# Performance work log

Measured on AMD Instinct MI355X. Metric: run time of the kernel, lower is better.

Reference implementation:

```python
import jax, jax.numpy as jnp
import numpy as np

B, R, C, O, I = 256, 1152, 10, 16, 8  # batch, routes, digit caps, out dim, in dim


def conv2d(x, w, b, stride, pad):
    y = jax.lax.conv_general_dilated(
        x, w, (stride, stride), ((pad, pad), (pad, pad)),
        dimension_numbers=("NCHW", "OIHW", "NCHW"))
    return y + b[None, :, None, None]


def maxpool2(x):
    # kernel 2, stride 2, padding 1 (torch pads with -inf for max pool)
    return jax.lax.reduce_window(
        x, -jnp.inf, jax.lax.max,
        (1, 1, 2, 2), (1, 1, 2, 2), ((0, 0), (0, 0), (1, 1), (1, 1)))


def squash(t):
    sn = (t ** 2).sum(-1, keepdims=True)
    return sn * t / ((1.0 + sn) * jnp.sqrt(sn))


def setup_inputs() -> dict:
    key = jax.random.key(0)
    ks = jax.random.split(key, 8)
    return {
        "data": jax.random.normal(ks[0], (B, 3, 76, 76), dtype=jnp.float32),
        "conv1_w": jax.random.normal(ks[1], (64, 3, 3, 3), dtype=jnp.float32) * 0.1,
        "conv1_b": jnp.zeros((64,), jnp.float32),
        "conv2_w": jax.random.normal(ks[2], (128, 64, 3, 3), dtype=jnp.float32) * 0.05,
        "conv2_b": jnp.zeros((128,), jnp.float32),
        "prim_w": jax.random.normal(ks[3], (8, 32, 128, 9, 9), dtype=jnp.float32) * 0.02,
        "prim_b": jnp.zeros((8, 32), jnp.float32),
        "W": jax.random.normal(ks[4], (R, C, O, I), dtype=jnp.float32),
        "cls_w1": jax.random.normal(ks[5], (10, 160, 100), dtype=jnp.float32) * 0.05,
        "cls_b1": jnp.zeros((10, 100), jnp.float32),
        "cls_w2": jax.random.normal(ks[6], (10, 100, 1), dtype=jnp.float32) * 0.05,
        "cls_b2": jnp.zeros((10, 1), jnp.float32),
    }


def reference(data, conv1_w, conv1_b, conv2_w, conv2_b, prim_w, prim_b, W,
              cls_w1, cls_b1, cls_w2, cls_b2):
    # ---- ConvLayer ----
    x = jax.nn.relu(conv2d(data, conv1_w, conv1_b, 1, 0))   # [B,64,74,74]
    x = maxpool2(x)                                          # [B,64,38,38]
    x = jax.nn.relu(conv2d(x, conv2_w, conv2_b, 1, 1))       # [B,128,38,38]
    x = maxpool2(x)                                          # [B,128,20,20]

    # ---- PrimaryCaps: 8 parallel convs fused into one grouped-by-output conv ----
    pw = prim_w.reshape(8 * 32, 128, 9, 9)
    pb = prim_b.reshape(8 * 32)
    u = conv2d(x, pw, pb, 2, 0)                              # [B,256,6,6]
    u = u.reshape(B, R, I)                                   # [B,1152,8] (same flatten order as torch view)
    u = squash(u)

    # ---- DigitCaps dynamic routing ----
    u_hat = jnp.einsum("rcoi,bri->brco", W, u)               # [B,R,C,O]
    b_ij = jnp.zeros((R, C), u_hat.dtype)
    v_j = None
    for it in range(3):
        c_ij = jax.nn.softmax(b_ij, axis=0)                  # softmax over routes (dim=1 in torch)
        s_j = jnp.einsum("rc,brco->bco", c_ij, u_hat)        # [B,C,O]
        # torch squashes over trailing singleton dim -> elementwise squash
        v_j = squash(s_j[..., None])[..., 0]                 # [B,C,O]
        if it < 2:
            a_ij = jnp.einsum("brco,bco->brc", u_hat, v_j).mean(0)  # [R,C]
            b_ij = b_ij + a_ij

    output = v_j[..., None]                                  # [B,10,16,1]

    # ---- 10 classifiers (Linear->ReLU->Linear->Sigmoid), batched over classifier idx k ----
    feat = output.reshape(B, -1)                             # [B,160]
    h = jax.nn.relu(jnp.einsum("bf,kfh->bkh", feat, cls_w1) + cls_b1)
    logits = jnp.einsum("bkh,kho->bko", h, cls_w2) + cls_b2  # [B,10,1]
    cls = jax.nn.sigmoid(logits)[..., 0]                     # [B,10]
    return (output, cls)
```

## Files before the change

kernel.cpp:

```cpp
#include <hip/hip_runtime.h>
#include <hip/hip_bf16.h>


typedef __bf16 bf16x8 __attribute__((ext_vector_type(8)));
typedef float  f32x4  __attribute__((ext_vector_type(4)));
typedef ushort u16x8  __attribute__((ext_vector_type(8)));

static __device__ __forceinline__ ushort f2bf(float f) {
    __hip_bfloat16 h = __float2bfloat16(f);
    return *(ushort*)&h;
}
static __device__ __forceinline__ float b2f(ushort u) {
    return __uint_as_float(((unsigned)u) << 16);
}

typedef __attribute__((address_space(1))) const unsigned int* as1_u32p;
typedef __attribute__((address_space(3))) unsigned int* as3_u32p;
static __device__ __forceinline__ void gl16(const void* g, void* l) {
    __builtin_amdgcn_global_load_lds((as1_u32p)g, (as3_u32p)l, 16, 0, 0);
}

__global__ __launch_bounds__(256) void k_prep_awt(
    const float* __restrict__ pw, __hip_bfloat16* __restrict__ Awt)
{
    __shared__ float ls[10368];
    const int oc = blockIdx.x;
    const int tid = threadIdx.x;
    const float* src = pw + oc * 10368;
    for (int i = tid; i < 10368; i += 256) ls[i] = src[i];
    __syncthreads();
    __hip_bfloat16* dst = Awt + oc * 10368;
    for (int o = tid; o < 10368; o += 256) {
        int k81 = o >> 7, ic = o & 127;
        dst[o] = __float2bfloat16(ls[ic * 81 + k81]);
    }
}

__global__ __launch_bounds__(256) void k_prep_wt(
    const float* __restrict__ W, __hip_bfloat16* __restrict__ Wt)
{
    __shared__ float ls[8 * 1281];
    const int r0 = blockIdx.x * 8;
    const int tid = threadIdx.x;
    const float* src = W + (size_t)r0 * 1280;
    for (int i = tid; i < 10240; i += 256) {
        int rr = i / 1280, rem = i - rr * 1280;
        ls[rr * 1281 + rem] = src[i];
    }
    __syncthreads();
    for (int o = tid; o < 10240; o += 256) {
        int co = o >> 6, rem = o & 63;
        int rr = rem >> 3, i = rem & 7;
        Wt[(size_t)co * 9216 + r0 * 8 + rem] =
            __float2bfloat16(ls[rr * 1281 + co * 8 + i]);
    }
}

__global__ __launch_bounds__(256) void k_prep_small(
    const float* __restrict__ w1, const float* __restrict__ w2,
    __hip_bfloat16* __restrict__ Aw1, __hip_bfloat16* __restrict__ Aw2)
{
    int t = blockIdx.x * 256 + threadIdx.x;
    if (t < 73728) {
        int oc = t / 576, rem = t % 576;
        int k9 = rem >> 6, ic = rem & 63;
        Aw2[t] = __float2bfloat16(w2[(oc * 64 + ic) * 9 + k9]);
    } else if (t < 75776) {
        int q = t - 73728;
        int oc = q >> 5, k = q & 31;
        Aw1[q] = __float2bfloat16(k < 27 ? w1[oc * 27 + k] : 0.f);
    }
}

__global__ __launch_bounds__(256) void k_conv1_mfma(
    const float* __restrict__ data, const __hip_bfloat16* __restrict__ Aw1,
    const float* __restrict__ b1, __hip_bfloat16* __restrict__ P1t)
{
    __shared__ float tile[960];
    const int tid = threadIdx.x;
    const int py = blockIdx.x % 38, b = blockIdx.x / 38;

    #pragma unroll
    for (int c = 0; c < 4; c++) {
        int idx = tid + c * 256;
        if (idx < 960) {
            float val = 0.f;
            if (idx < 936) {
                int ic = idx / 312, rem = idx % 312;
                int rl = rem / 78, lc = rem % 78;
                int ri = 2 * py - 1 + rl, xi = lc - 1;
                if ((unsigned)ri < 76u && (unsigned)xi < 76u)
                    val = data[(b * 3 + ic) * 5776 + ri * 76 + xi];
            }
            tile[idx] = val;
        }
    }

    const int wave = tid >> 6, lane = tid & 63;
    const int l15 = lane & 15, quad = lane >> 4;

    bf16x8 af = *(const bf16x8*)((const ushort*)Aw1 + (wave * 16 + l15) * 32 + quad * 8);

    int koff[8]; bool kok[8];
    #pragma unroll
    for (int j = 0; j < 8; j++) {
        int kk = quad * 8 + j;
        kok[j] = kk < 27;
        int ic = kk / 9, rem = kk - ic * 9, ky = rem / 3, kx = rem - ky * 3;
        koff[j] = kok[j] ? (ic * 312 + ky * 78 + kx) : 0;
    }

    float bias[4];
    #pragma unroll
    for (int r = 0; r < 4; r++) bias[r] = b1[wave * 16 + quad * 4 + r];

    const bool valid0 = (py > 0);
    const bool valid1 = (py < 37);

    __syncthreads();

    #pragma unroll
    for (int t5 = 0; t5 < 5; t5++) {
        int n_x = t5 * 16 + l15;
        bool col_ok = (unsigned)(n_x - 1) < 74u;

        bf16x8 bf0, bf1;
        #pragma unroll
        for (int j = 0; j < 8; j++) {
            float v0 = tile[koff[j] + n_x];
            float v1 = tile[koff[j] + 78 + n_x];
            bool ok = col_ok && kok[j];
            bf0[j] = (__bf16)(ok ? v0 : 0.f);
            bf1[j] = (__bf16)(ok ? v1 : 0.f);
        }
        f32x4 z = {0.f, 0.f, 0.f, 0.f};
        f32x4 c0 = __builtin_amdgcn_mfma_f32_16x16x32_bf16(af, bf0, z, 0, 0, 0);
        f32x4 c1 = __builtin_amdgcn_mfma_f32_16x16x32_bf16(af, bf1, z, 0, 0, 0);

        f32x4 p;
        #pragma unroll
        for (int r = 0; r < 4; r++) {
            float r0 = (valid0 && col_ok) ? fmaxf(c0[r] + bias[r], 0.f) : 0.f;
            float r1 = (valid1 && col_ok) ? fmaxf(c1[r] + bias[r], 0.f) : 0.f;
            p[r] = fmaxf(r0, r1);
        }
        #pragma unroll
        for (int r = 0; r < 4; r++)
            p[r] = fmaxf(p[r], __shfl_xor(p[r], 1));

        if (!(l15 & 1)) {
            int px = t5 * 8 + (l15 >> 1);
            if (px < 38) {
                ushort4 pk;
                pk.x = f2bf(p[0]); pk.y = f2bf(p[1]);
                pk.z = f2bf(p[2]); pk.w = f2bf(p[3]);
                *(ushort4*)((ushort*)P1t + ((size_t)(b * 38 + py) * 38 + px) * 64
                            + wave * 16 + quad * 4) = pk;
            }
        }
    }
}

__global__ __launch_bounds__(256, 4) void k_conv2_pool_mfma(
    const __hip_bfloat16* __restrict__ P1t,
    const __hip_bfloat16* __restrict__ Aw2,
    const float* __restrict__ cb,
    const ushort* __restrict__ zpage,
    __hip_bfloat16* __restrict__ P2t)
{
    __shared__ ushort lA[128 * 64];
    __shared__ ushort lB[128 * 64];
    const int tid  = threadIdx.x;
    const int grp  = blockIdx.x / 50, toff = blockIdx.x % 50;
    const int wave = tid >> 6, lane = tid & 63;
    const int wm   = wave & 1, wn = wave >> 1;
    const int lane15 = lane & 15, quad = lane >> 4;

    const int sl = ((lane & 7) ^ (lane >> 3)) * 8;

    int oA[4], oB[4], yv[4], xv[4];
    #pragma unroll
    for (int i = 0; i < 4; i++) {
        int row = wave * 32 + i * 8 + (lane >> 3);
        oA[i] = row * 576 + sl;
        int off = toff * 128 + row;
        int bb = off / 1600, rem = off % 1600;
        int cell = rem >> 2, q = rem & 3;
        int py = cell / 20, px = cell % 20;
        int y = 2 * py - 1 + (q >> 1), x = 2 * px - 1 + (q & 1);
        yv[i] = y; xv[i] = x;
        oB[i] = (((grp * 4 + bb) * 38 + (y - 1)) * 38 + (x - 1)) * 64 + sl;
    }
    ushort* lAq = &lA[wave * 2048];
    ushort* lBq = &lB[wave * 2048];

    const int s7 = lane15 & 7;
    const int c0 = (quad ^ s7) * 8;
    const int c1 = ((quad + 4) ^ s7) * 8;
    const ushort* aRd0 = &lA[(wm * 64 + lane15) * 64 + c0];
    const ushort* aRd1 = &lA[(wm * 64 + lane15) * 64 + c1];
    const ushort* bRd0 = &lB[(wn * 64 + lane15) * 64 + c0];
    const ushort* bRd1 = &lB[(wn * 64 + lane15) * 64 + c1];

    f32x4 zero = {0.f, 0.f, 0.f, 0.f};
    f32x4 acc[4][4];
    #pragma unroll
    for (int i = 0; i < 4; i++)
        #pragma unroll
        for (int j = 0; j < 4; j++) acc[i][j] = zero;

    for (int kb = 0; kb < 9; kb++) {
        int ky = kb / 3, kx = kb - ky * 3;
        int dB = (ky * 38 + kx) << 6;
        int dA = kb << 6;

        __syncthreads();
        #pragma unroll
        for (int i = 0; i < 4; i++) {
            gl16((const ushort*)Aw2 + oA[i] + dA, lAq + i * 512);
            bool ok = ((unsigned)(yv[i] - 1 + ky) < 38u) &&
                      ((unsigned)(xv[i] - 1 + kx) < 38u);
            const ushort* src = ok ? ((const ushort*)P1t + (ptrdiff_t)(oB[i] + dB))
                                   : (zpage + sl);
            gl16(src, lBq + i * 512);
        }
        __syncthreads();

        #pragma unroll
        for (int kk = 0; kk < 2; kk++) {
            const ushort* ap = kk ? aRd1 : aRd0;
            const ushort* bp = kk ? bRd1 : bRd0;
            bf16x8 af[4], bf[4];
            #pragma unroll
            for (int tm = 0; tm < 4; tm++)
                af[tm] = *(const bf16x8*)(ap + tm * 1024);
            #pragma unroll
            for (int tn = 0; tn < 4; tn++)
                bf[tn] = *(const bf16x8*)(bp + tn * 1024);
            #pragma unroll
            for (int tm = 0; tm < 4; tm++)
                #pragma unroll
                for (int tn = 0; tn < 4; tn++)
                    acc[tm][tn] = __builtin_amdgcn_mfma_f32_16x16x32_bf16(
                        af[tm], bf[tn], acc[tm][tn], 0, 0, 0);
        }
    }

    #pragma unroll
    for (int tn = 0; tn < 4; tn++) {
        int woff = toff * 128 + wn * 64 + tn * 16 + lane15;
        int ebb = woff / 1600, erem = woff % 1600;
        int ecell = erem >> 2, eq = erem & 3;
        int epy = ecell / 20, epx = ecell % 20;
        int ey = 2 * epy - 1 + (eq >> 1), ex = 2 * epx - 1 + (eq & 1);
        bool vq = ((unsigned)ey < 38u) && ((unsigned)ex < 38u);
        int eb = grp * 4 + ebb;
        #pragma unroll
        for (int tm = 0; tm < 4; tm++) {
            int m0 = wm * 64 + tm * 16 + quad * 4;
            f32x4 a = acc[tm][tn];
            f32x4 p;
            #pragma unroll
            for (int r = 0; r < 4; r++)
                p[r] = vq ? fmaxf(a[r] + cb[m0 + r], 0.f) : 0.f;
            #pragma unroll
            for (int r = 0; r < 4; r++) {
                p[r] = fmaxf(p[r], __shfl_xor(p[r], 1));
                p[r] = fmaxf(p[r], __shfl_xor(p[r], 2));
            }
            if (eq == 0) {
                ushort4 pk;
                pk.x = f2bf(p[0]); pk.y = f2bf(p[1]);
                pk.z = f2bf(p[2]); pk.w = f2bf(p[3]);
                *(ushort4*)((ushort*)P2t + (((size_t)eb * 20 + epy) * 20 + epx) * 128 + m0) = pk;
            }
        }
    }
}

__global__ __launch_bounds__(256, 4) void k_primcaps_mfma(
    const __hip_bfloat16* __restrict__ P2t,
    const __hip_bfloat16* __restrict__ Awt,
    float* __restrict__ partU)
{
    __shared__ ushort lA[128 * 64];
    __shared__ ushort lB[128 * 64];
    const int tid  = threadIdx.x;
    const int chunk = blockIdx.x / 144;
    const int tile  = blockIdx.x % 144;
    const int bm   = tile & 1;
    const int bn   = tile >> 1;
    const int wave = tid >> 6, lane = tid & 63;
    const int wm   = wave & 1, wn = wave >> 1;
    const int lane15 = lane & 15, quad = lane >> 4;

    const int sl = ((lane & 7) ^ (lane >> 3)) * 8;

    int oA[4], oB[4];
    #pragma unroll
    for (int i = 0; i < 4; i++) {
        int row = wave * 32 + i * 8 + (lane >> 3);
        oA[i] = (bm * 128 + row) * 10368 + sl;
        int n = bn * 128 + row;
        int cbn = n / 36, cs = n % 36;
        int cy = cs / 6, cx = cs % 6;
        oB[i] = ((cbn * 20 + 2 * cy) * 20 + 2 * cx) * 128 + sl;
    }
    ushort* lAq = &lA[wave * 2048];
    ushort* lBq = &lB[wave * 2048];

    const int s7 = lane15 & 7;
    const int c0 = (quad ^ s7) * 8;
    const int c1 = ((quad + 4) ^ s7) * 8;
    const ushort* aRd0 = &lA[(wm * 64 + lane15) * 64 + c0];
    const ushort* aRd1 = &lA[(wm * 64 + lane15) * 64 + c1];
    const ushort* bRd0 = &lB[(wn * 64 + lane15) * 64 + c0];
    const ushort* bRd1 = &lB[(wn * 64 + lane15) * 64 + c1];

    f32x4 zero = {0.f, 0.f, 0.f, 0.f};
    f32x4 acc[4][4];
    #pragma unroll
    for (int i = 0; i < 4; i++)
        #pragma unroll
        for (int j = 0; j < 4; j++) acc[i][j] = zero;

    const int kb0 = chunk * 27;
    for (int ki = 0; ki < 27; ki++) {
        int kb = kb0 + ki;
        int k81 = kb >> 1;
        int ky = k81 / 9, kx = k81 - ky * 9;
        int dB = (ky * 20 + kx) * 128 + (kb & 1) * 64;
        int dA = kb << 6;

        __syncthreads();
        #pragma unroll
        for (int i = 0; i < 4; i++) {
            gl16((const ushort*)Awt + (size_t)oA[i] + dA, lAq + i * 512);
            gl16((const ushort*)P2t + oB[i] + dB, lBq + i * 512);
        }
        __syncthreads();

        #pragma unroll
        for (int kk = 0; kk < 2; kk++) {
            const ushort* ap = kk ? aRd1 : aRd0;
            const ushort* bp = kk ? bRd1 : bRd0;
            bf16x8 af[4], bf[4];
            #pragma unroll
            for (int tm = 0; tm < 4; tm++)
                af[tm] = *(const bf16x8*)(ap + tm * 1024);
            #pragma unroll
            for (int tn = 0; tn < 4; tn++)
                bf[tn] = *(const bf16x8*)(bp + tn * 1024);
            #pragma unroll
            for (int tm = 0; tm < 4; tm++)
                #pragma unroll
                for (int tn = 0; tn < 4; tn++)
                    acc[tm][tn] = __builtin_amdgcn_mfma_f32_16x16x32_bf16(
                        af[tm], bf[tn], acc[tm][tn], 0, 0, 0);
        }
    }

    float* base = partU + chunk * 2359296;
    #pragma unroll
    for (int tm = 0; tm < 4; tm++) {
        int m0 = bm * 128 + wm * 64 + tm * 16 + quad * 4;
        #pragma unroll
        for (int tn = 0; tn < 4; tn++) {
            int nn = bn * 128 + wn * 64 + tn * 16 + lane15;
            int ob = nn / 36, os = nn % 36;
            float* up = base + ob * 9216 + os;
            f32x4 a = acc[tm][tn];
            #pragma unroll
            for (int r = 0; r < 4; r++)
                up[(m0 + r) * 36] = a[r];
        }
    }
}

__global__ __launch_bounds__(256) void k_reduce_squash(
    const float* __restrict__ partU, const float* __restrict__ pb,
    ushort* __restrict__ u_bf)
{
    int t = blockIdx.x * 256 + threadIdx.x;
    float4 a = {0.f, 0.f, 0.f, 0.f}, b4 = {0.f, 0.f, 0.f, 0.f};
    #pragma unroll
    for (int p = 0; p < 6; p++) {
        const float4* pp = (const float4*)(partU + p * 2359296 + t * 8);
        float4 x = pp[0], y = pp[1];
        a.x += x.x; a.y += x.y; a.z += x.z; a.w += x.w;
        b4.x += y.x; b4.y += y.y; b4.z += y.z; b4.w += y.w;
    }
    int lb = (t % 1152) * 8;
    int oc0 = lb / 36, s0 = lb - oc0 * 36;
    float vals[8] = {a.x, a.y, a.z, a.w, b4.x, b4.y, b4.z, b4.w};
    float sn = 0.f;
    #pragma unroll
    for (int e = 0; e < 8; e++) {
        int oc = oc0 + ((s0 + e) >= 36 ? 1 : 0);
        vals[e] += pb[oc];
        sn += vals[e] * vals[e];
    }
    float sc = sqrtf(sn) / (1.f + sn);
    u16x8 o8;
    #pragma unroll
    for (int e = 0; e < 8; e++) o8[e] = f2bf(vals[e] * sc);
    *(u16x8*)(u_bf + (size_t)t * 8) = o8;
}

__global__ __launch_bounds__(320) void k_sj_fused(
    const ushort* __restrict__ u_bf,
    const __hip_bfloat16* __restrict__ Wt,
    const float* __restrict__ expb,
    float* __restrict__ partS,
    int iter)
{
    __shared__ ushort ush[8 * 576];
    __shared__ float cf[720];
    __shared__ float sred[320];
    __shared__ float sinv[10];
    const int tid = threadIdx.x;
    const int bt = blockIdx.x & 31, kc = blockIdx.x >> 5;
    const int co = tid % 160, half = tid / 160;

    if (iter > 0) {
        int c = tid % 10, g = tid / 10;
        float s = 0.f;
        for (int r = g; r < 1152; r += 32) s += expb[r * 10 + c];
        sred[tid] = s;
        for (int i = tid; i < 720; i += 320) cf[i] = expb[kc * 720 + i];
        __syncthreads();
        if (tid < 10) {
            float t2 = 0.f;
            #pragma unroll
            for (int gg = 0; gg < 32; gg++) t2 += sred[tid + gg * 10];
            sinv[tid] = 1.f / t2;
        }
    }
    for (int i = tid; i < 576; i += 320)
        ((uint4*)ush)[i] = ((const uint4*)u_bf)[(size_t)(bt * 8 + (i / 72)) * 1152
                                                + kc * 72 + (i % 72)];
    __syncthreads();

    const int cc = co >> 4;
    const float scl = (iter > 0) ? sinv[cc] : 0.f;
    const float cuni = 1.f / 1152.f;
    const ushort* wp = (const ushort*)Wt + (size_t)co * 9216 + kc * 576 + half * 288;

    float acc[8] = {0.f, 0.f, 0.f, 0.f, 0.f, 0.f, 0.f, 0.f};
    for (int rr = 0; rr < 36; rr++) {
        float cl = (iter == 0) ? cuni : cf[(half * 36 + rr) * 10 + cc] * scl;
        u16x8 wq = *(const u16x8*)(wp + rr * 8);
        float wv[8];
        #pragma unroll
        for (int ii = 0; ii < 8; ii++)
            wv[ii] = b2f(wq[ii]) * cl;
        int kbase = half * 288 + rr * 8;
        #pragma unroll
        for (int bb = 0; bb < 8; bb++) {
            u16x8 uq = *(const u16x8*)&ush[bb * 576 + kbase];
            #pragma unroll
            for (int ii = 0; ii < 8; ii++)
                acc[bb] += wv[ii] * b2f(uq[ii]);
        }
    }
    float* ps = partS + (kc * 2 + half) * 40960;
    #pragma unroll
    for (int bb = 0; bb < 8; bb++)
        ps[(bt * 8 + bb) * 160 + co] = acc[bb];
}

__global__ __launch_bounds__(320) void k_vj_cls(
    const float* __restrict__ partS, float* __restrict__ v,
    const float* __restrict__ w1, const float* __restrict__ b1,
    const float* __restrict__ w2, const float* __restrict__ b2,
    float* __restrict__ out, int write_out)
{
    const int b = blockIdx.x;
    const int tid = threadIdx.x;
    __shared__ float feat[160];
    if (tid < 160) {
        float s = 0.f;
        #pragma unroll
        for (int p = 0; p < 32; p++) s += partS[p * 40960 + b * 160 + tid];
        float vv = s * fabsf(s) / (1.f + s * s);
        v[b * 160 + tid] = vv;
        feat[tid] = vv;
        if (write_out) out[b * 160 + tid] = vv;
    }
    if (!write_out) return;
    __syncthreads();
    int k = tid >> 5, j = tid & 31;
    float acc = 0.f;
    for (int h = j; h < 100; h += 32) {
        float a = b1[k * 100 + h];
        for (int f = 0; f < 160; f++) a += feat[f] * w1[(k * 160 + f) * 100 + h];
        acc += fmaxf(a, 0.f) * w2[k * 100 + h];
    }
    #pragma unroll
    for (int d = 16; d > 0; d >>= 1) acc += __shfl_xor(acc, d);
    if (j == 0)
        out[40960 + b * 10 + k] = 1.f / (1.f + expf(-(acc + b2[k])));
}

__global__ __launch_bounds__(320) void k_mmat_aij(
    const ushort* __restrict__ u_bf, const float* __restrict__ v,
    const float* __restrict__ W, float* __restrict__ bij,
    float* __restrict__ expb)
{
    const int r = blockIdx.x;
    const int tid = threadIdx.x;
    const int co = tid % 160, bh = tid / 160;
    float acc[8] = {0.f, 0.f, 0.f, 0.f, 0.f, 0.f, 0.f, 0.f};
    for (int b = bh; b < 256; b += 2) {
        float vv = v[b * 160 + co];
        u16x8 uq = *(const u16x8*)(u_bf + (size_t)b * 9216 + r * 8);
        #pragma unroll
        for (int j = 0; j < 8; j++) acc[j] += vv * b2f(uq[j]);
    }
    __shared__ float red[2560];
    __shared__ float Ml[8][160];
    #pragma unroll
    for (int j = 0; j < 8; j++) red[j * 320 + bh * 160 + co] = acc[j];
    __syncthreads();
    if (tid < 160) {
        #pragma unroll
        for (int j = 0; j < 8; j++)
            Ml[j][tid] = (red[j * 320 + tid] + red[j * 320 + 160 + tid]) * (1.f / 256.f);
    }
    __syncthreads();
    int c = tid >> 5, j32 = tid & 31;
    const float* wr = W + ((size_t)r * 10 + c) * 128;
    float a2 = 0.f;
    #pragma unroll
    for (int m = 0; m < 4; m++) {
        int idx = j32 + m * 32;
        int o = idx >> 3, i = idx & 7;
        a2 += wr[idx] * Ml[i][c * 16 + o];
    }
    #pragma unroll
    for (int d = 16; d > 0; d >>= 1) a2 += __shfl_xor(a2, d);
    if (j32 == 0) {
        float nb = bij[c * 1152 + r] + a2;
        bij[c * 1152 + r] = nb;
        expb[r * 10 + c] = expf(nb);
    }
}

extern "C" void kernel_launch(void* const* d_in, const int* in_sizes, int n_in,
                              void* d_out, int out_size, void* d_ws, size_t ws_size,
                              hipStream_t stream) {
    const float* data    = (const float*)d_in[0];
    const float* conv1_w = (const float*)d_in[1];
    const float* conv1_b = (const float*)d_in[2];
    const float* conv2_w = (const float*)d_in[3];
    const float* conv2_b = (const float*)d_in[4];
    const float* prim_w  = (const float*)d_in[5];
    const float* prim_b  = (const float*)d_in[6];
    const float* W       = (const float*)d_in[7];
    const float* cls_w1  = (const float*)d_in[8];
    const float* cls_b1  = (const float*)d_in[9];
    const float* cls_w2  = (const float*)d_in[10];
    const float* cls_b2  = (const float*)d_in[11];
    float* out = (float*)d_out;

    char* ws = (char*)d_ws;
    float*          partU = (float*)(ws + 0);
    __hip_bfloat16* P2t   = (__hip_bfloat16*)(ws + 56623104);
    ushort*         zpage = (ushort*)(ws + 69730304);
    __hip_bfloat16* P1t   = (__hip_bfloat16*)(ws + 94633984);
    __hip_bfloat16* Awt   = (__hip_bfloat16*)(ws + 141950976);
    __hip_bfloat16* Wt    = (__hip_bfloat16*)(ws + 147259392);
    ushort*         u_bf  = (ushort*)(ws + 150208512);
    float*          partS = (float*)(ws + 154927104);
    float*          v     = (float*)(ws + 163446784);
    float*          bij   = (float*)(ws + 163610624);
    float*          expb  = (float*)(ws + 163656704);
    __hip_bfloat16* Aw2   = (__hip_bfloat16*)(ws + 163702784);
    __hip_bfloat16* Aw1   = (__hip_bfloat16*)(ws + 163850240);

    hipMemsetAsync(bij, 0, 11520 * sizeof(float), stream);
    hipMemsetAsync(zpage, 0, 128, stream);

    k_prep_awt<<<256, 256, 0, stream>>>(prim_w, Awt);
    k_prep_wt<<<144, 256, 0, stream>>>(W, Wt);
    k_prep_small<<<296, 256, 0, stream>>>(conv1_w, conv2_w, Aw1, Aw2);
    k_conv1_mfma<<<9728, 256, 0, stream>>>(data, Aw1, conv1_b, P1t);
    k_conv2_pool_mfma<<<3200, 256, 0, stream>>>(P1t, Aw2, conv2_b, zpage, P2t);
    k_primcaps_mfma<<<864, 256, 0, stream>>>(P2t, Awt, partU);
    k_reduce_squash<<<1152, 256, 0, stream>>>(partU, prim_b, u_bf);

    for (int it = 0; it < 3; it++) {
        k_sj_fused<<<512, 320, 0, stream>>>(u_bf, Wt, expb, partS, it);
        k_vj_cls<<<256, 320, 0, stream>>>(partS, v, cls_w1, cls_b1, cls_w2,
                                          cls_b2, out, it == 2 ? 1 : 0);
        if (it < 2)
            k_mmat_aij<<<1152, 320, 0, stream>>>(u_bf, v, W, bij, expb);
    }
}
```

Baseline: 563.4 us.

## Fuse weight prep kernels and coalesce conv2 and primary-caps output stores

```diff
diff --git a/kernel.cpp b/kernel.cpp
--- a/kernel.cpp
+++ b/kernel.cpp
@@ -20,55 +20,50 @@
     __builtin_amdgcn_global_load_lds((as1_u32p)g, (as3_u32p)l, 16, 0, 0);
 }
 
-__global__ __launch_bounds__(256) void k_prep_awt(
-    const float* __restrict__ pw, __hip_bfloat16* __restrict__ Awt)
+__global__ __launch_bounds__(256) void k_prep_fused(
+    const float* __restrict__ w1, const float* __restrict__ w2,
+    const float* __restrict__ pw, const float* __restrict__ W,
+    __hip_bfloat16* __restrict__ Aw1, __hip_bfloat16* __restrict__ Aw2,
+    __hip_bfloat16* __restrict__ Awt, __hip_bfloat16* __restrict__ Wt)
 {
     __shared__ float ls[10368];
-    const int oc = blockIdx.x;
+    const int bid = blockIdx.x;
     const int tid = threadIdx.x;
-    const float* src = pw + oc * 10368;
-    for (int i = tid; i < 10368; i += 256) ls[i] = src[i];
-    __syncthreads();
-    __hip_bfloat16* dst = Awt + oc * 10368;
-    for (int o = tid; o < 10368; o += 256) {
-        int k81 = o >> 7, ic = o & 127;
-        dst[o] = __float2bfloat16(ls[ic * 81 + k81]);
-    }
-}
-
-__global__ __launch_bounds__(256) void k_prep_wt(
-    const float* __restrict__ W, __hip_bfloat16* __restrict__ Wt)
-{
-    __shared__ float ls[8 * 1281];
-    const int r0 = blockIdx.x * 8;
-    const int tid = threadIdx.x;
-    const float* src = W + (size_t)r0 * 1280;
-    for (int i = tid; i < 10240; i += 256) {
-        int rr = i / 1280, rem = i - rr * 1280;
-        ls[rr * 1281 + rem] = src[i];
-    }
-    __syncthreads();
-    for (int o = tid; o < 10240; o += 256) {
-        int co = o >> 6, rem = o & 63;
-        int rr = rem >> 3, i = rem & 7;
-        Wt[(size_t)co * 9216 + r0 * 8 + rem] =
-            __float2bfloat16(ls[rr * 1281 + co * 8 + i]);
-    }
-}
-
-__global__ __launch_bounds__(256) void k_prep_small(
-    const float* __restrict__ w1, const float* __restrict__ w2,
-    __hip_bfloat16* __restrict__ Aw1, __hip_bfloat16* __restrict__ Aw2)
-{
-    int t = blockIdx.x * 256 + threadIdx.x;
-    if (t < 73728) {
-        int oc = t / 576, rem = t % 576;
-        int k9 = rem >> 6, ic = rem & 63;
-        Aw2[t] = __float2bfloat16(w2[(oc * 64 + ic) * 9 + k9]);
-    } else if (t < 75776) {
-        int q = t - 73728;
-        int oc = q >> 5, k = q & 31;
-        Aw1[q] = __float2bfloat16(k < 27 ? w1[oc * 27 + k] : 0.f);
+    if (bid < 256) {
+        const int oc = bid;
+        const float* src = pw + oc * 10368;
+        for (int i = tid; i < 10368; i += 256) ls[i] = src[i];
+        __syncthreads();
+        __hip_bfloat16* dst = Awt + oc * 10368;
+        for (int o = tid; o < 10368; o += 256) {
+            int k81 = o >> 7, ic = o & 127;
+            dst[o] = __float2bfloat16(ls[ic * 81 + k81]);
+        }
+    } else if (bid < 400) {
+        const int r0 = (bid - 256) * 8;
+        const float* src = W + (size_t)r0 * 1280;
+        for (int i = tid; i < 10240; i += 256) {
+            int rr = i / 1280, rem = i - rr * 1280;
+            ls[rr * 1281 + rem] = src[i];
+        }
+        __syncthreads();
+        for (int o = tid; o < 10240; o += 256) {
+            int co = o >> 6, rem = o & 63;
+            int rr = rem >> 3, i = rem & 7;
+            Wt[(size_t)co * 9216 + r0 * 8 + rem] =
+                __float2bfloat16(ls[rr * 1281 + co * 8 + i]);
+        }
+    } else {
+        int t = (bid - 400) * 256 + tid;
+        if (t < 73728) {
+            int oc = t / 576, rem = t % 576;
+            int k9 = rem >> 6, ic = rem & 63;
+            Aw2[t] = __float2bfloat16(w2[(oc * 64 + ic) * 9 + k9]);
+        } else if (t < 75776) {
+            int q = t - 73728;
+            int oc = q >> 5, k = q & 31;
+            Aw1[q] = __float2bfloat16(k < 27 ? w1[oc * 27 + k] : 0.f);
+        }
     }
 }
 
@@ -246,6 +241,8 @@
         }
     }
 
+    __syncthreads();
+    ushort* lout = lA;
     #pragma unroll
     for (int tn = 0; tn < 4; tn++) {
         int woff = toff * 128 + wn * 64 + tn * 16 + lane15;
@@ -254,7 +251,7 @@
         int epy = ecell / 20, epx = ecell % 20;
         int ey = 2 * epy - 1 + (eq >> 1), ex = 2 * epx - 1 + (eq & 1);
         bool vq = ((unsigned)ey < 38u) && ((unsigned)ex < 38u);
-        int eb = grp * 4 + ebb;
+        int c32 = wn * 16 + tn * 4 + (lane15 >> 2);
         #pragma unroll
         for (int tm = 0; tm < 4; tm++) {
             int m0 = wm * 64 + tm * 16 + quad * 4;
@@ -272,9 +269,23 @@
                 ushort4 pk;
                 pk.x = f2bf(p[0]); pk.y = f2bf(p[1]);
                 pk.z = f2bf(p[2]); pk.w = f2bf(p[3]);
-                *(ushort4*)((ushort*)P2t + (((size_t)eb * 20 + epy) * 20 + epx) * 128 + m0) = pk;
+                *(ushort4*)(lout + c32 * 128 + m0) = pk;
             }
         }
+    }
+    __syncthreads();
+    {
+        int c32 = tid >> 3, part = tid & 7;
+        int woff = toff * 128 + c32 * 4;
+        int ebb = woff / 1600, erem = woff % 1600;
+        int ecell = erem >> 2;
+        int epy = ecell / 20, epx = ecell % 20;
+        int eb = grp * 4 + ebb;
+        const uint4* src = (const uint4*)(lout + c32 * 128 + part * 16);
+        uint4* dst = (uint4*)((ushort*)P2t
+                     + (((size_t)eb * 20 + epy) * 20 + epx) * 128 + part * 16);
+        dst[0] = src[0];
+        dst[1] = src[1];
     }
 }
 
@@ -360,19 +371,17 @@
         }
     }
 
-    float* base = partU + chunk * 2359296;
+    float* base = partU + (size_t)chunk * 2359296;
     #pragma unroll
     for (int tm = 0; tm < 4; tm++) {
         int m0 = bm * 128 + wm * 64 + tm * 16 + quad * 4;
         #pragma unroll
         for (int tn = 0; tn < 4; tn++) {
             int nn = bn * 128 + wn * 64 + tn * 16 + lane15;
-            int ob = nn / 36, os = nn % 36;
-            float* up = base + ob * 9216 + os;
             f32x4 a = acc[tm][tn];
             #pragma unroll
             for (int r = 0; r < 4; r++)
-                up[(m0 + r) * 36] = a[r];
+                base[(size_t)(m0 + r) * 9216 + nn] = a[r];
         }
     }
 }
@@ -382,17 +391,26 @@
     ushort* __restrict__ u_bf)
 {
     int t = blockIdx.x * 256 + threadIdx.x;
-    float4 a = {0.f, 0.f, 0.f, 0.f}, b4 = {0.f, 0.f, 0.f, 0.f};
-    #pragma unroll
-    for (int p = 0; p < 6; p++) {
-        const float4* pp = (const float4*)(partU + p * 2359296 + t * 8);
-        float4 x = pp[0], y = pp[1];
-        a.x += x.x; a.y += x.y; a.z += x.z; a.w += x.w;
-        b4.x += y.x; b4.y += y.y; b4.z += y.z; b4.w += y.w;
-    }
+    int b = t / 1152;
     int lb = (t % 1152) * 8;
     int oc0 = lb / 36, s0 = lb - oc0 * 36;
-    float vals[8] = {a.x, a.y, a.z, a.w, b4.x, b4.y, b4.z, b4.w};
+    float vals[8] = {0.f, 0.f, 0.f, 0.f, 0.f, 0.f, 0.f, 0.f};
+    #pragma unroll
+    for (int p = 0; p < 6; p++) {
+        const float* base = partU + (size_t)p * 2359296;
+        if (s0 <= 28) {
+            const float4* pp = (const float4*)(base + (size_t)oc0 * 9216 + b * 36 + s0);
+            float4 x = pp[0], y = pp[1];
+            vals[0] += x.x; vals[1] += x.y; vals[2] += x.z; vals[3] += x.w;
+            vals[4] += y.x; vals[5] += y.y; vals[6] += y.z; vals[7] += y.w;
+        } else {
+            const float4* pa = (const float4*)(base + (size_t)oc0 * 9216 + b * 36 + 32);
+            const float4* pbq = (const float4*)(base + (size_t)(oc0 + 1) * 9216 + b * 36);
+            float4 x = pa[0], y = pbq[0];
+            vals[0] += x.x; vals[1] += x.y; vals[2] += x.z; vals[3] += x.w;
+            vals[4] += y.x; vals[5] += y.y; vals[6] += y.z; vals[7] += y.w;
+        }
+    }
     float sn = 0.f;
     #pragma unroll
     for (int e = 0; e < 8; e++) {
@@ -581,9 +599,8 @@
     hipMemsetAsync(bij, 0, 11520 * sizeof(float), stream);
     hipMemsetAsync(zpage, 0, 128, stream);
 
-    k_prep_awt<<<256, 256, 0, stream>>>(prim_w, Awt);
-    k_prep_wt<<<144, 256, 0, stream>>>(W, Wt);
-    k_prep_small<<<296, 256, 0, stream>>>(conv1_w, conv2_w, Aw1, Aw2);
+    k_prep_fused<<<696, 256, 0, stream>>>(conv1_w, conv2_w, prim_w, W,
+                                          Aw1, Aw2, Awt, Wt);
     k_conv1_mfma<<<9728, 256, 0, stream>>>(data, Aw1, conv1_b, P1t);
     k_conv2_pool_mfma<<<3200, 256, 0, stream>>>(P1t, Aw2, conv2_b, zpage, P2t);
     k_primcaps_mfma<<<864, 256, 0, stream>>>(P2t, Awt, partU);
```

Result: faster. 550.9 us (-2.2%).
